# Optimization experiments

Measured on AMD Instinct MI355X. Metric: run time of the kernel, lower is better.

Reference implementation:

```python
import jax, jax.numpy as jnp
import numpy as np

B, T, C, H = 4, 4096, 1024, 64


def setup_inputs() -> dict:
    key = jax.random.key(0)
    kx, kk, kq, kv = jax.random.split(key, 4)
    x = jax.random.normal(kx, (B, T, C), dtype=jnp.float32)
    # bias-free linear weights, stored as [in, out] so y = x @ W
    Wk = jax.random.normal(kk, (C, H), dtype=jnp.float32) * (C ** -0.5)
    Wq = jax.random.normal(kq, (C, H), dtype=jnp.float32) * (C ** -0.5)
    Wv = jax.random.normal(kv, (C, H), dtype=jnp.float32) * (C ** -0.5)
    return {"x": x, "Wk": Wk, "Wq": Wq, "Wv": Wv}


def reference(x, Wk, Wq, Wv):
    b, t, c = x.shape
    k = x @ Wk  # [B,T,H]
    q = x @ Wq
    v = x @ Wv
    # NOTE: original scales by C**-0.5 (num_embed), not head_size**-0.5
    wei = jnp.einsum('bqh,bkh->bqk', q, k) * (c ** -0.5)  # [B,T,T]
    causal = jnp.tril(jnp.ones((t, t), dtype=bool))
    wei = jnp.where(causal, wei, -jnp.inf)
    wei = jax.nn.softmax(wei, axis=-1)
    # dropout p=0.0 (eval) -> identity
    return jnp.einsum('bqk,bkh->bqh', wei, v)  # [B,T,H]
```

## Files before the change

### kernel.cpp

```cpp
#include <hip/hip_runtime.h>
#include <hip/hip_bf16.h>

typedef unsigned short u16;
typedef unsigned int u32;
using f32x4 = __attribute__((ext_vector_type(4))) float;
using s16x8 = __attribute__((ext_vector_type(8))) short;

#define BATCH 4
#define SEQ   4096
#define CDIM  1024
#define HDIM  64
#define QT_N  256

__device__ inline u16 f32_to_bf16(float f) {
    u32 u = __builtin_bit_cast(u32, f);
    u += 0x7FFFu + ((u >> 16) & 1u);
    return (u16)(u >> 16);
}
__device__ inline u32 pkbf16(float a, float b) {
    return (u32)f32_to_bf16(a) | ((u32)f32_to_bf16(b) << 16);
}
__device__ inline f32x4 mfma16(s16x8 a, s16x8 b, f32x4 c) {
    return __builtin_amdgcn_mfma_f32_16x16x32_bf16(a, b, c, 0, 0, 0);
}


__global__ __launch_bounds__(64) void wtrans_kernel(
        const float* __restrict__ Wk, const float* __restrict__ Wq,
        const float* __restrict__ Wv, u16* __restrict__ Wtf) {
    int bx = blockIdx.x;
    int nt = bx >> 5, kc = bx & 31;
    int lane = threadIdx.x;
    int l16 = lane & 15, qd = lane >> 4;
    int n = nt * 16 + l16;
    int a = n >> 6, h = n & 63;
    const float* src = (a == 0) ? Wk : (a == 1) ? Wq : Wv;
    float scale = (a == 1) ? 0.045084220027780106f : 1.0f;
    u32 p[4];
#pragma unroll
    for (int pp = 0; pp < 4; ++pp) {
        int k = kc * 32 + qd * 8 + pp * 2;
        p[pp] = pkbf16(src[k * HDIM + h] * scale, src[(k + 1) * HDIM + h] * scale);
    }
    uint4 u; u.x = p[0]; u.y = p[1]; u.z = p[2]; u.w = p[3];
    *(uint4*)&Wtf[(size_t)((nt * 32 + kc) * 64 + lane) * 8] = u;
}

__global__ __launch_bounds__(256, 2) void proj_kernel(
        const float* __restrict__ x, const u16* __restrict__ Wtf,
        u16* __restrict__ qf, u16* __restrict__ kf, u16* __restrict__ vf) {
    __shared__ __align__(16) u16 xs[32][1032];
    int t = threadIdx.x, lane = t & 63, w = t >> 6;
    int quad = lane >> 4, l16 = lane & 15;
    int row0 = blockIdx.x * 32;

    const float* xb = x + (size_t)row0 * CDIM;
#pragma unroll 4
    for (int i = 0; i < 32; ++i) {
        float4 f = *(const float4*)(xb + (size_t)i * CDIM + t * 4);
        uint2 u; u.x = pkbf16(f.x, f.y); u.y = pkbf16(f.z, f.w);
        *(uint2*)&xs[i][t * 4] = u;
    }
    __syncthreads();

    f32x4 acc[2][3];
#pragma unroll
    for (int m = 0; m < 2; ++m)
#pragma unroll
        for (int n = 0; n < 3; ++n) acc[m][n] = (f32x4){0.f, 0.f, 0.f, 0.f};

#pragma unroll 4
    for (int kc = 0; kc < 32; ++kc) {
        s16x8 a0 = *(const s16x8*)&xs[l16][kc * 32 + quad * 8];
        s16x8 a1 = *(const s16x8*)&xs[16 + l16][kc * 32 + quad * 8];
#pragma unroll
        for (int n = 0; n < 3; ++n) {
            int nt = w * 3 + n;
            s16x8 b = *(const s16x8*)&Wtf[(size_t)((nt * 32 + kc) * 64 + lane) * 8];
            acc[0][n] = mfma16(a0, b, acc[0][n]);
            acc[1][n] = mfma16(a1, b, acc[1][n]);
        }
    }
#pragma unroll
    for (int m = 0; m < 2; ++m) {
        int rbase = row0 + m * 16 + quad * 4;
        int bb = rbase >> 12, rl = rbase & 4095;
#pragma unroll
        for (int n = 0; n < 3; ++n) {
            int n0 = w * 48 + n * 16;
            if (n0 < 128) {
                u16* dst = (n0 < 64) ? kf : qf;
                int h = (n0 & 63) + l16;
                int tt16 = rl >> 4, hc = h >> 5, qd2 = (h >> 3) & 3, j = h & 7;
                size_t base = ((size_t)((bb * 256 + tt16) * 2 + hc) * 64
                               + qd2 * 16 + (rl & 15)) * 8 + j;
#pragma unroll
                for (int r = 0; r < 4; ++r)
                    dst[base + (size_t)r * 8] = f32_to_bf16(acc[m][n][r]);
            } else {
                int h0 = n0 - 128;
                int ht = h0 >> 4;
                int kc2 = rl >> 5, qdv = (rl >> 3) & 3, j0 = rl & 7;
                u32 lo = pkbf16(acc[m][n][0], acc[m][n][1]);
                u32 hi = pkbf16(acc[m][n][2], acc[m][n][3]);
                size_t base = ((size_t)((bb * 128 + kc2) * 4 + ht) * 64
                               + qdv * 16 + l16) * 8 + j0;
                uint2 u; u.x = lo; u.y = hi;
                *(uint2*)&vf[base] = u;
            }
        }
    }
}

__global__ __launch_bounds__(256, 4) void flash_kernel(
        const u16* __restrict__ qf, const u16* __restrict__ kf,
        const u16* __restrict__ vf, float* __restrict__ out) {
    __shared__ float cb[4][16][68];
    __shared__ float lb[4][16];
    int t = threadIdx.x, w = t >> 6, lane = t & 63;
    int quad = lane >> 4, l16 = lane & 15;
    int qt = (int)gridDim.x - 1 - (int)blockIdx.x;
    int b = blockIdx.y;

    const u16* qp = qf + ((size_t)(b * QT_N + qt) * 2 * 64 + lane) * 8;
    s16x8 bq0 = *(const s16x8*)qp;
    s16x8 bq1 = *(const s16x8*)(qp + 64 * 8);
    s16x8 ones;
#pragma unroll
    for (int j = 0; j < 8; ++j) ones[j] = (short)0x3F80;

    f32x4 o[4], o5 = (f32x4){0.f, 0.f, 0.f, 0.f};
#pragma unroll
    for (int i = 0; i < 4; ++i) o[i] = (f32x4){0.f, 0.f, 0.f, 0.f};

    int nb = (qt * 16 + 16 + 63) >> 6;
    int iters = (nb + 3) >> 2;
    int rowq = qt * 16 + l16;
    const u16* kfb = kf + (size_t)b * 256 * 2 * 512;
    const u16* vfb = vf + (size_t)b * 128 * 4 * 512;
    int a0 = ((quad & 1) * 32 + l16) * 4;
    int a1 = a0 + 64;
    u32 msk = (quad < 2) ? 0xFFFFFFFFu : 0u;

    auto iteration = [&](int kb, bool domask) {
        int kt0 = kb * 4;
        f32x4 sT[4];
#pragma unroll
        for (int kt = 0; kt < 4; ++kt) {
            const u16* kp = kfb + ((size_t)(kt0 + kt) * 2 * 64 + lane) * 8;
            s16x8 k0 = *(const s16x8*)kp;
            s16x8 k1 = *(const s16x8*)(kp + 64 * 8);
            f32x4 s = (f32x4){0.f, 0.f, 0.f, 0.f};
            s = mfma16(k0, bq0, s);
            s = mfma16(k1, bq1, s);
            sT[kt] = s;
        }
        u32 P01[4], P23[4];
#pragma unroll
        for (int kt = 0; kt < 4; ++kt) {
            float e[4];
#pragma unroll
            for (int r = 0; r < 4; ++r) {
                float ev = __builtin_amdgcn_exp2f(sT[kt][r]);
                if (domask) {
                    int key = kb * 64 + kt * 16 + quad * 4 + r;
                    ev = (key > rowq) ? 0.f : ev;
                }
                e[r] = ev;
            }
            P01[kt] = pkbf16(e[0], e[1]);
            P23[kt] = pkbf16(e[2], e[3]);
        }
#pragma unroll
        for (int c = 0; c < 2; ++c) {
            int t0 = 2 * c, t1 = 2 * c + 1;
            u32 x0 = (u32)__builtin_amdgcn_ds_bpermute(a0, (int)P01[t0]);
            u32 y0 = (u32)__builtin_amdgcn_ds_bpermute(a0, (int)P01[t1]);
            u32 x1 = (u32)__builtin_amdgcn_ds_bpermute(a0, (int)P23[t0]);
            u32 y1 = (u32)__builtin_amdgcn_ds_bpermute(a0, (int)P23[t1]);
            u32 x2 = (u32)__builtin_amdgcn_ds_bpermute(a1, (int)P01[t0]);
            u32 y2 = (u32)__builtin_amdgcn_ds_bpermute(a1, (int)P01[t1]);
            u32 x3 = (u32)__builtin_amdgcn_ds_bpermute(a1, (int)P23[t0]);
            u32 y3 = (u32)__builtin_amdgcn_ds_bpermute(a1, (int)P23[t1]);
            uint4 pu;
            pu.x = (x0 & msk) | (y0 & ~msk);
            pu.y = (x1 & msk) | (y1 & ~msk);
            pu.z = (x2 & msk) | (y2 & ~msk);
            pu.w = (x3 & msk) | (y3 & ~msk);
            s16x8 pb = __builtin_bit_cast(s16x8, pu);
#pragma unroll
            for (int ht = 0; ht < 4; ++ht) {
                s16x8 vA = *(const s16x8*)&vfb[((size_t)((kb * 2 + c) * 4 + ht) * 64
                                                + lane) * 8];
                o[ht] = mfma16(vA, pb, o[ht]);
            }
            o5 = mfma16(ones, pb, o5);
        }
    };

    for (int i = 0; i < iters - 1; ++i) iteration(4 * i + w, false);
    {
        int kb = 4 * (iters - 1) + w;
        if (kb < nb) iteration(kb, true);
    }
#pragma unroll
    for (int ht = 0; ht < 4; ++ht)
#pragma unroll
        for (int r = 0; r < 4; ++r)
            cb[w][l16][ht * 16 + quad * 4 + r] = o[ht][r];
    if (quad == 0) lb[w][l16] = o5[0];
    __syncthreads();
    int row = t >> 4, c0 = (t & 15) * 4;
    float l = lb[0][row] + lb[1][row] + lb[2][row] + lb[3][row];
    float4 s0 = *(const float4*)&cb[0][row][c0];
    float4 s1 = *(const float4*)&cb[1][row][c0];
    float4 s2 = *(const float4*)&cb[2][row][c0];
    float4 s3 = *(const float4*)&cb[3][row][c0];
    float4 r;
    r.x = (s0.x + s1.x + s2.x + s3.x) / l;
    r.y = (s0.y + s1.y + s2.y + s3.y) / l;
    r.z = (s0.z + s1.z + s2.z + s3.z) / l;
    r.w = (s0.w + s1.w + s2.w + s3.w) / l;
    *(float4*)&out[((size_t)(b * SEQ) + qt * 16 + row) * HDIM + c0] = r;
}

extern "C" void kernel_launch(void* const* d_in, const int* in_sizes, int n_in,
                              void* d_out, int out_size, void* d_ws, size_t ws_size,
                              hipStream_t stream) {
    const float* x  = (const float*)d_in[0];
    const float* Wk = (const float*)d_in[1];
    const float* Wq = (const float*)d_in[2];
    const float* Wv = (const float*)d_in[3];
    u16* wsu = (u16*)d_ws;
    u16* Wtf = wsu;
    u16* kf  = Wtf + 196608;
    u16* qf  = kf + 1048576;
    u16* vf  = qf + 1048576;
    float* out = (float*)d_out;

    hipLaunchKernelGGL(wtrans_kernel, dim3(384), dim3(64), 0, stream, Wk, Wq, Wv, Wtf);
    hipLaunchKernelGGL(proj_kernel, dim3(512), dim3(256), 0, stream, x, Wtf, qf, kf, vf);
    hipLaunchKernelGGL(flash_kernel, dim3(QT_N, BATCH), dim3(256), 0, stream, qf, kf, vf, out);
}
```

Before: 145.3 us.

## Process two 16-row query tiles per block to reuse K/V loads

Each flash block now handles 32 query rows (two 16-row tiles) instead of 16, so every K and V fragment loaded from global memory feeds two sets of MFMAs. The grid is halved and the epilogue reduces 32 rows, using a reciprocal multiply instead of divides. This cuts K/V traffic per query roughly in half. In exchange it adds register pressure from doubled accumulators and score tiles, gives coarser causal load balance, and the diagonal block masks more wasted work.

```diff
diff --git a/kernel.cpp b/kernel.cpp
--- a/kernel.cpp
+++ b/kernel.cpp
@@ -115,27 +115,35 @@
 __global__ __launch_bounds__(256, 4) void flash_kernel(
         const u16* __restrict__ qf, const u16* __restrict__ kf,
         const u16* __restrict__ vf, float* __restrict__ out) {
-    __shared__ float cb[4][16][68];
-    __shared__ float lb[4][16];
+    __shared__ float cb[4][32][68];
+    __shared__ float lb[4][32];
     int t = threadIdx.x, w = t >> 6, lane = t & 63;
     int quad = lane >> 4, l16 = lane & 15;
-    int qt = (int)gridDim.x - 1 - (int)blockIdx.x;
+    int qt2 = (int)gridDim.x - 1 - (int)blockIdx.x;
     int b = blockIdx.y;
 
-    const u16* qp = qf + ((size_t)(b * QT_N + qt) * 2 * 64 + lane) * 8;
-    s16x8 bq0 = *(const s16x8*)qp;
-    s16x8 bq1 = *(const s16x8*)(qp + 64 * 8);
+    const u16* qp0 = qf + ((size_t)((b * QT_N + qt2 * 2) * 2) * 64 + lane) * 8;
+    const u16* qp1 = qp0 + 2 * 64 * 8;
+    s16x8 bq[2][2];
+    bq[0][0] = *(const s16x8*)qp0;
+    bq[0][1] = *(const s16x8*)(qp0 + 512);
+    bq[1][0] = *(const s16x8*)qp1;
+    bq[1][1] = *(const s16x8*)(qp1 + 512);
     s16x8 ones;
 #pragma unroll
     for (int j = 0; j < 8; ++j) ones[j] = (short)0x3F80;
 
-    f32x4 o[4], o5 = (f32x4){0.f, 0.f, 0.f, 0.f};
-#pragma unroll
-    for (int i = 0; i < 4; ++i) o[i] = (f32x4){0.f, 0.f, 0.f, 0.f};
-
-    int nb = (qt * 16 + 16 + 63) >> 6;
+    f32x4 o[2][4], o5[2];
+#pragma unroll
+    for (int tl = 0; tl < 2; ++tl) {
+        o5[tl] = (f32x4){0.f, 0.f, 0.f, 0.f};
+#pragma unroll
+        for (int i = 0; i < 4; ++i) o[tl][i] = (f32x4){0.f, 0.f, 0.f, 0.f};
+    }
+
+    int nb = (qt2 * 32 + 32 + 63) >> 6;
     int iters = (nb + 3) >> 2;
-    int rowq = qt * 16 + l16;
+    int rowq0 = qt2 * 32 + l16;
     const u16* kfb = kf + (size_t)b * 256 * 2 * 512;
     const u16* vfb = vf + (size_t)b * 128 * 4 * 512;
     int a0 = ((quad & 1) * 32 + l16) * 4;
@@ -143,58 +151,65 @@
     u32 msk = (quad < 2) ? 0xFFFFFFFFu : 0u;
 
     auto iteration = [&](int kb, bool domask) {
-        int kt0 = kb * 4;
-        f32x4 sT[4];
+        f32x4 sT[2][4];
 #pragma unroll
         for (int kt = 0; kt < 4; ++kt) {
-            const u16* kp = kfb + ((size_t)(kt0 + kt) * 2 * 64 + lane) * 8;
+            const u16* kp = kfb + ((size_t)((kb * 4 + kt) * 2) * 64 + lane) * 8;
             s16x8 k0 = *(const s16x8*)kp;
-            s16x8 k1 = *(const s16x8*)(kp + 64 * 8);
-            f32x4 s = (f32x4){0.f, 0.f, 0.f, 0.f};
-            s = mfma16(k0, bq0, s);
-            s = mfma16(k1, bq1, s);
-            sT[kt] = s;
-        }
-        u32 P01[4], P23[4];
-#pragma unroll
-        for (int kt = 0; kt < 4; ++kt) {
-            float e[4];
-#pragma unroll
-            for (int r = 0; r < 4; ++r) {
-                float ev = __builtin_amdgcn_exp2f(sT[kt][r]);
-                if (domask) {
-                    int key = kb * 64 + kt * 16 + quad * 4 + r;
-                    ev = (key > rowq) ? 0.f : ev;
+            s16x8 k1 = *(const s16x8*)(kp + 512);
+            f32x4 z = (f32x4){0.f, 0.f, 0.f, 0.f};
+            sT[0][kt] = mfma16(k1, bq[0][1], mfma16(k0, bq[0][0], z));
+            sT[1][kt] = mfma16(k1, bq[1][1], mfma16(k0, bq[1][0], z));
+        }
+        u32 P01[2][4], P23[2][4];
+#pragma unroll
+        for (int tl = 0; tl < 2; ++tl) {
+            int rowq = rowq0 + tl * 16;
+#pragma unroll
+            for (int kt = 0; kt < 4; ++kt) {
+                float e[4];
+#pragma unroll
+                for (int r = 0; r < 4; ++r) {
+                    float ev = __builtin_amdgcn_exp2f(sT[tl][kt][r]);
+                    if (domask) {
+                        int key = kb * 64 + kt * 16 + quad * 4 + r;
+                        ev = (key > rowq) ? 0.f : ev;
+                    }
+                    e[r] = ev;
                 }
-                e[r] = ev;
+                P01[tl][kt] = pkbf16(e[0], e[1]);
+                P23[tl][kt] = pkbf16(e[2], e[3]);
             }
-            P01[kt] = pkbf16(e[0], e[1]);
-            P23[kt] = pkbf16(e[2], e[3]);
         }
 #pragma unroll
         for (int c = 0; c < 2; ++c) {
+            s16x8 vA[4];
+#pragma unroll
+            for (int ht = 0; ht < 4; ++ht)
+                vA[ht] = *(const s16x8*)&vfb[((size_t)((kb * 2 + c) * 4 + ht) * 64
+                                             + lane) * 8];
             int t0 = 2 * c, t1 = 2 * c + 1;
-            u32 x0 = (u32)__builtin_amdgcn_ds_bpermute(a0, (int)P01[t0]);
-            u32 y0 = (u32)__builtin_amdgcn_ds_bpermute(a0, (int)P01[t1]);
-            u32 x1 = (u32)__builtin_amdgcn_ds_bpermute(a0, (int)P23[t0]);
-            u32 y1 = (u32)__builtin_amdgcn_ds_bpermute(a0, (int)P23[t1]);
-            u32 x2 = (u32)__builtin_amdgcn_ds_bpermute(a1, (int)P01[t0]);
-            u32 y2 = (u32)__builtin_amdgcn_ds_bpermute(a1, (int)P01[t1]);
-            u32 x3 = (u32)__builtin_amdgcn_ds_bpermute(a1, (int)P23[t0]);
-            u32 y3 = (u32)__builtin_amdgcn_ds_bpermute(a1, (int)P23[t1]);
-            uint4 pu;
-            pu.x = (x0 & msk) | (y0 & ~msk);
-            pu.y = (x1 & msk) | (y1 & ~msk);
-            pu.z = (x2 & msk) | (y2 & ~msk);
-            pu.w = (x3 & msk) | (y3 & ~msk);
-            s16x8 pb = __builtin_bit_cast(s16x8, pu);
-#pragma unroll
-            for (int ht = 0; ht < 4; ++ht) {
-                s16x8 vA = *(const s16x8*)&vfb[((size_t)((kb * 2 + c) * 4 + ht) * 64
-                                                + lane) * 8];
-                o[ht] = mfma16(vA, pb, o[ht]);
+#pragma unroll
+            for (int tl = 0; tl < 2; ++tl) {
+                u32 x0 = (u32)__builtin_amdgcn_ds_bpermute(a0, (int)P01[tl][t0]);
+                u32 y0 = (u32)__builtin_amdgcn_ds_bpermute(a0, (int)P01[tl][t1]);
+                u32 x1 = (u32)__builtin_amdgcn_ds_bpermute(a0, (int)P23[tl][t0]);
+                u32 y1 = (u32)__builtin_amdgcn_ds_bpermute(a0, (int)P23[tl][t1]);
+                u32 x2 = (u32)__builtin_amdgcn_ds_bpermute(a1, (int)P01[tl][t0]);
+                u32 y2 = (u32)__builtin_amdgcn_ds_bpermute(a1, (int)P01[tl][t1]);
+                u32 x3 = (u32)__builtin_amdgcn_ds_bpermute(a1, (int)P23[tl][t0]);
+                u32 y3 = (u32)__builtin_amdgcn_ds_bpermute(a1, (int)P23[tl][t1]);
+                uint4 pu;
+                pu.x = (x0 & msk) | (y0 & ~msk);
+                pu.y = (x1 & msk) | (y1 & ~msk);
+                pu.z = (x2 & msk) | (y2 & ~msk);
+                pu.w = (x3 & msk) | (y3 & ~msk);
+                s16x8 pb = __builtin_bit_cast(s16x8, pu);
+#pragma unroll
+                for (int ht = 0; ht < 4; ++ht)
+                    o[tl][ht] = mfma16(vA[ht], pb, o[tl][ht]);
+                o5[tl] = mfma16(ones, pb, o5[tl]);
             }
-            o5 = mfma16(ones, pb, o5);
         }
     };
 
@@ -204,24 +219,31 @@
         if (kb < nb) iteration(kb, true);
     }
 #pragma unroll
-    for (int ht = 0; ht < 4; ++ht)
-#pragma unroll
-        for (int r = 0; r < 4; ++r)
-            cb[w][l16][ht * 16 + quad * 4 + r] = o[ht][r];
-    if (quad == 0) lb[w][l16] = o5[0];
+    for (int tl = 0; tl < 2; ++tl) {
+#pragma unroll
+        for (int ht = 0; ht < 4; ++ht)
+#pragma unroll
+            for (int r = 0; r < 4; ++r)
+                cb[w][tl * 16 + l16][ht * 16 + quad * 4 + r] = o[tl][ht][r];
+        if (quad == 0) lb[w][tl * 16 + l16] = o5[tl][0];
+    }
     __syncthreads();
-    int row = t >> 4, c0 = (t & 15) * 4;
+    int row = t >> 3, c0 = (t & 7) * 8;
     float l = lb[0][row] + lb[1][row] + lb[2][row] + lb[3][row];
-    float4 s0 = *(const float4*)&cb[0][row][c0];
-    float4 s1 = *(const float4*)&cb[1][row][c0];
-    float4 s2 = *(const float4*)&cb[2][row][c0];
-    float4 s3 = *(const float4*)&cb[3][row][c0];
-    float4 r;
-    r.x = (s0.x + s1.x + s2.x + s3.x) / l;
-    r.y = (s0.y + s1.y + s2.y + s3.y) / l;
-    r.z = (s0.z + s1.z + s2.z + s3.z) / l;
-    r.w = (s0.w + s1.w + s2.w + s3.w) / l;
-    *(float4*)&out[((size_t)(b * SEQ) + qt * 16 + row) * HDIM + c0] = r;
+    float rcp = 1.0f / l;
+    float4 s0 = (float4){0.f, 0.f, 0.f, 0.f}, s1 = s0;
+#pragma unroll
+    for (int w4 = 0; w4 < 4; ++w4) {
+        float4 p0 = *(const float4*)&cb[w4][row][c0];
+        float4 p1 = *(const float4*)&cb[w4][row][c0 + 4];
+        s0.x += p0.x; s0.y += p0.y; s0.z += p0.z; s0.w += p0.w;
+        s1.x += p1.x; s1.y += p1.y; s1.z += p1.z; s1.w += p1.w;
+    }
+    s0.x *= rcp; s0.y *= rcp; s0.z *= rcp; s0.w *= rcp;
+    s1.x *= rcp; s1.y *= rcp; s1.z *= rcp; s1.w *= rcp;
+    float* op = &out[((size_t)(b * SEQ) + qt2 * 32 + row) * HDIM + c0];
+    *(float4*)op = s0;
+    *(float4*)(op + 4) = s1;
 }
 
 extern "C" void kernel_launch(void* const* d_in, const int* in_sizes, int n_in,
@@ -240,5 +262,5 @@
 
     hipLaunchKernelGGL(wtrans_kernel, dim3(384), dim3(64), 0, stream, Wk, Wq, Wv, Wtf);
     hipLaunchKernelGGL(proj_kernel, dim3(512), dim3(256), 0, stream, x, Wtf, qf, kf, vf);
-    hipLaunchKernelGGL(flash_kernel, dim3(QT_N, BATCH), dim3(256), 0, stream, qf, kf, vf, out);
-}
+    hipLaunchKernelGGL(flash_kernel, dim3(SEQ / 32, BATCH), dim3(256), 0, stream, qf, kf, vf, out);
+}
```

New measurement: 147.2 us. Within noise of the previous version (+1.3%).

## Split key blocks across eight waves and halve projection row tile

Applied to the files above, without the earlier changes.

The flash kernel now uses 512 threads, so eight waves share one query tile's key range instead of four, and the final cross-wave reduction is widened to match. V operand loads are hoisted ahead of the bpermute shuffles so they overlap. The projection kernel processes 16 rows per block with twice as many blocks, which raises occupancy and spreads the work more evenly. In exchange, the larger reduction costs more shared memory, and each wave does less work per tile on short causal rows.

```diff
diff --git a/kernel.cpp b/kernel.cpp
--- a/kernel.cpp
+++ b/kernel.cpp
@@ -46,85 +46,78 @@
     *(uint4*)&Wtf[(size_t)((nt * 32 + kc) * 64 + lane) * 8] = u;
 }
 
-__global__ __launch_bounds__(256, 2) void proj_kernel(
+__global__ __launch_bounds__(256, 4) void proj_kernel(
         const float* __restrict__ x, const u16* __restrict__ Wtf,
         u16* __restrict__ qf, u16* __restrict__ kf, u16* __restrict__ vf) {
-    __shared__ __align__(16) u16 xs[32][1032];
+    __shared__ __align__(16) u16 xs[16][1032];
     int t = threadIdx.x, lane = t & 63, w = t >> 6;
     int quad = lane >> 4, l16 = lane & 15;
-    int row0 = blockIdx.x * 32;
+    int row0 = blockIdx.x * 16;
 
     const float* xb = x + (size_t)row0 * CDIM;
 #pragma unroll 4
-    for (int i = 0; i < 32; ++i) {
+    for (int i = 0; i < 16; ++i) {
         float4 f = *(const float4*)(xb + (size_t)i * CDIM + t * 4);
         uint2 u; u.x = pkbf16(f.x, f.y); u.y = pkbf16(f.z, f.w);
         *(uint2*)&xs[i][t * 4] = u;
     }
     __syncthreads();
 
-    f32x4 acc[2][3];
-#pragma unroll
-    for (int m = 0; m < 2; ++m)
-#pragma unroll
-        for (int n = 0; n < 3; ++n) acc[m][n] = (f32x4){0.f, 0.f, 0.f, 0.f};
+    f32x4 acc[3];
+#pragma unroll
+    for (int n = 0; n < 3; ++n) acc[n] = (f32x4){0.f, 0.f, 0.f, 0.f};
 
 #pragma unroll 4
     for (int kc = 0; kc < 32; ++kc) {
         s16x8 a0 = *(const s16x8*)&xs[l16][kc * 32 + quad * 8];
-        s16x8 a1 = *(const s16x8*)&xs[16 + l16][kc * 32 + quad * 8];
 #pragma unroll
         for (int n = 0; n < 3; ++n) {
             int nt = w * 3 + n;
             s16x8 b = *(const s16x8*)&Wtf[(size_t)((nt * 32 + kc) * 64 + lane) * 8];
-            acc[0][n] = mfma16(a0, b, acc[0][n]);
-            acc[1][n] = mfma16(a1, b, acc[1][n]);
-        }
-    }
-#pragma unroll
-    for (int m = 0; m < 2; ++m) {
-        int rbase = row0 + m * 16 + quad * 4;
-        int bb = rbase >> 12, rl = rbase & 4095;
-#pragma unroll
-        for (int n = 0; n < 3; ++n) {
-            int n0 = w * 48 + n * 16;
-            if (n0 < 128) {
-                u16* dst = (n0 < 64) ? kf : qf;
-                int h = (n0 & 63) + l16;
-                int tt16 = rl >> 4, hc = h >> 5, qd2 = (h >> 3) & 3, j = h & 7;
-                size_t base = ((size_t)((bb * 256 + tt16) * 2 + hc) * 64
-                               + qd2 * 16 + (rl & 15)) * 8 + j;
-#pragma unroll
-                for (int r = 0; r < 4; ++r)
-                    dst[base + (size_t)r * 8] = f32_to_bf16(acc[m][n][r]);
-            } else {
-                int h0 = n0 - 128;
-                int ht = h0 >> 4;
-                int kc2 = rl >> 5, qdv = (rl >> 3) & 3, j0 = rl & 7;
-                u32 lo = pkbf16(acc[m][n][0], acc[m][n][1]);
-                u32 hi = pkbf16(acc[m][n][2], acc[m][n][3]);
-                size_t base = ((size_t)((bb * 128 + kc2) * 4 + ht) * 64
-                               + qdv * 16 + l16) * 8 + j0;
-                uint2 u; u.x = lo; u.y = hi;
-                *(uint2*)&vf[base] = u;
-            }
-        }
-    }
-}
-
-__global__ __launch_bounds__(256, 4) void flash_kernel(
+            acc[n] = mfma16(a0, b, acc[n]);
+        }
+    }
+    int rbase = row0 + quad * 4;
+    int bb = rbase >> 12, rl = rbase & 4095;
+#pragma unroll
+    for (int n = 0; n < 3; ++n) {
+        int n0 = w * 48 + n * 16;
+        if (n0 < 128) {
+            u16* dst = (n0 < 64) ? kf : qf;
+            int h = (n0 & 63) + l16;
+            int tt16 = rl >> 4, hc = h >> 5, qd2 = (h >> 3) & 3, j = h & 7;
+            size_t base = ((size_t)((bb * 256 + tt16) * 2 + hc) * 64
+                           + qd2 * 16 + (rl & 15)) * 8 + j;
+#pragma unroll
+            for (int r = 0; r < 4; ++r)
+                dst[base + (size_t)r * 8] = f32_to_bf16(acc[n][r]);
+        } else {
+            int h0 = n0 - 128;
+            int ht = h0 >> 4;
+            int kc2 = rl >> 5, qdv = (rl >> 3) & 3, j0 = rl & 7;
+            u32 lo = pkbf16(acc[n][0], acc[n][1]);
+            u32 hi = pkbf16(acc[n][2], acc[n][3]);
+            size_t base = ((size_t)((bb * 128 + kc2) * 4 + ht) * 64
+                           + qdv * 16 + l16) * 8 + j0;
+            uint2 u; u.x = lo; u.y = hi;
+            *(uint2*)&vf[base] = u;
+        }
+    }
+}
+
+__global__ __launch_bounds__(512, 8) void flash_kernel(
         const u16* __restrict__ qf, const u16* __restrict__ kf,
         const u16* __restrict__ vf, float* __restrict__ out) {
-    __shared__ float cb[4][16][68];
-    __shared__ float lb[4][16];
+    __shared__ float cb[8][16][68];
+    __shared__ float lb[8][16];
     int t = threadIdx.x, w = t >> 6, lane = t & 63;
     int quad = lane >> 4, l16 = lane & 15;
     int qt = (int)gridDim.x - 1 - (int)blockIdx.x;
     int b = blockIdx.y;
 
-    const u16* qp = qf + ((size_t)(b * QT_N + qt) * 2 * 64 + lane) * 8;
+    const u16* qp = qf + ((size_t)((b * QT_N + qt) * 2) * 64 + lane) * 8;
     s16x8 bq0 = *(const s16x8*)qp;
-    s16x8 bq1 = *(const s16x8*)(qp + 64 * 8);
+    s16x8 bq1 = *(const s16x8*)(qp + 512);
     s16x8 ones;
 #pragma unroll
     for (int j = 0; j < 8; ++j) ones[j] = (short)0x3F80;
@@ -134,7 +127,7 @@
     for (int i = 0; i < 4; ++i) o[i] = (f32x4){0.f, 0.f, 0.f, 0.f};
 
     int nb = (qt * 16 + 16 + 63) >> 6;
-    int iters = (nb + 3) >> 2;
+    int iters = (nb + 7) >> 3;
     int rowq = qt * 16 + l16;
     const u16* kfb = kf + (size_t)b * 256 * 2 * 512;
     const u16* vfb = vf + (size_t)b * 128 * 4 * 512;
@@ -143,17 +136,14 @@
     u32 msk = (quad < 2) ? 0xFFFFFFFFu : 0u;
 
     auto iteration = [&](int kb, bool domask) {
-        int kt0 = kb * 4;
         f32x4 sT[4];
 #pragma unroll
         for (int kt = 0; kt < 4; ++kt) {
-            const u16* kp = kfb + ((size_t)(kt0 + kt) * 2 * 64 + lane) * 8;
+            const u16* kp = kfb + ((size_t)((kb * 4 + kt) * 2) * 64 + lane) * 8;
             s16x8 k0 = *(const s16x8*)kp;
-            s16x8 k1 = *(const s16x8*)(kp + 64 * 8);
-            f32x4 s = (f32x4){0.f, 0.f, 0.f, 0.f};
-            s = mfma16(k0, bq0, s);
-            s = mfma16(k1, bq1, s);
-            sT[kt] = s;
+            s16x8 k1 = *(const s16x8*)(kp + 512);
+            f32x4 z = (f32x4){0.f, 0.f, 0.f, 0.f};
+            sT[kt] = mfma16(k1, bq1, mfma16(k0, bq0, z));
         }
         u32 P01[4], P23[4];
 #pragma unroll
@@ -173,6 +163,11 @@
         }
 #pragma unroll
         for (int c = 0; c < 2; ++c) {
+            s16x8 vA[4];
+#pragma unroll
+            for (int ht = 0; ht < 4; ++ht)
+                vA[ht] = *(const s16x8*)&vfb[((size_t)((kb * 2 + c) * 4 + ht) * 64
+                                             + lane) * 8];
             int t0 = 2 * c, t1 = 2 * c + 1;
             u32 x0 = (u32)__builtin_amdgcn_ds_bpermute(a0, (int)P01[t0]);
             u32 y0 = (u32)__builtin_amdgcn_ds_bpermute(a0, (int)P01[t1]);
@@ -189,18 +184,15 @@
             pu.w = (x3 & msk) | (y3 & ~msk);
             s16x8 pb = __builtin_bit_cast(s16x8, pu);
 #pragma unroll
-            for (int ht = 0; ht < 4; ++ht) {
-                s16x8 vA = *(const s16x8*)&vfb[((size_t)((kb * 2 + c) * 4 + ht) * 64
-                                                + lane) * 8];
-                o[ht] = mfma16(vA, pb, o[ht]);
-            }
+            for (int ht = 0; ht < 4; ++ht)
+                o[ht] = mfma16(vA[ht], pb, o[ht]);
             o5 = mfma16(ones, pb, o5);
         }
     };
 
-    for (int i = 0; i < iters - 1; ++i) iteration(4 * i + w, false);
+    for (int i = 0; i < iters - 1; ++i) iteration(8 * i + w, false);
     {
-        int kb = 4 * (iters - 1) + w;
+        int kb = 8 * (iters - 1) + w;
         if (kb < nb) iteration(kb, true);
     }
 #pragma unroll
@@ -210,18 +202,17 @@
             cb[w][l16][ht * 16 + quad * 4 + r] = o[ht][r];
     if (quad == 0) lb[w][l16] = o5[0];
     __syncthreads();
-    int row = t >> 4, c0 = (t & 15) * 4;
-    float l = lb[0][row] + lb[1][row] + lb[2][row] + lb[3][row];
-    float4 s0 = *(const float4*)&cb[0][row][c0];
-    float4 s1 = *(const float4*)&cb[1][row][c0];
-    float4 s2 = *(const float4*)&cb[2][row][c0];
-    float4 s3 = *(const float4*)&cb[3][row][c0];
-    float4 r;
-    r.x = (s0.x + s1.x + s2.x + s3.x) / l;
-    r.y = (s0.y + s1.y + s2.y + s3.y) / l;
-    r.z = (s0.z + s1.z + s2.z + s3.z) / l;
-    r.w = (s0.w + s1.w + s2.w + s3.w) / l;
-    *(float4*)&out[((size_t)(b * SEQ) + qt * 16 + row) * HDIM + c0] = r;
+    int row = t >> 5, c0 = (t & 31) * 2;
+    float l = 0.f, s0 = 0.f, s1 = 0.f;
+#pragma unroll
+    for (int w8 = 0; w8 < 8; ++w8) {
+        l += lb[w8][row];
+        s0 += cb[w8][row][c0];
+        s1 += cb[w8][row][c0 + 1];
+    }
+    float rcp = 1.0f / l;
+    float2 rr; rr.x = s0 * rcp; rr.y = s1 * rcp;
+    *(float2*)&out[((size_t)(b * SEQ) + qt * 16 + row) * HDIM + c0] = rr;
 }
 
 extern "C" void kernel_launch(void* const* d_in, const int* in_sizes, int n_in,
@@ -239,6 +230,6 @@
     float* out = (float*)d_out;
 
     hipLaunchKernelGGL(wtrans_kernel, dim3(384), dim3(64), 0, stream, Wk, Wq, Wv, Wtf);
-    hipLaunchKernelGGL(proj_kernel, dim3(512), dim3(256), 0, stream, x, Wtf, qf, kf, vf);
-    hipLaunchKernelGGL(flash_kernel, dim3(QT_N, BATCH), dim3(256), 0, stream, qf, kf, vf, out);
-}
+    hipLaunchKernelGGL(proj_kernel, dim3(1024), dim3(256), 0, stream, x, Wtf, qf, kf, vf);
+    hipLaunchKernelGGL(flash_kernel, dim3(QT_N, BATCH), dim3(512), 0, stream, qf, kf, vf, out);
+}
```

Result: slower. 156.7 us (+7.8%).
